# Kernel optimization log

Measured on AMD Instinct MI355X. Metric: run time of the kernel, lower is better.

Reference implementation:

```python
import jax, jax.numpy as jnp
import numpy as np

B, NQ, NKV, D, H = 2, 2048, 2048, 2048, 16
HD = D // H


def setup_inputs() -> dict:
    key = jax.random.key(0)
    ks = jax.random.split(key, 9)
    return {
        "x": jax.random.normal(ks[0], (B, NQ, D), jnp.float32),
        "k": jax.random.normal(ks[1], (B, H, NKV, HD), jnp.float32),
        "v": jax.random.normal(ks[2], (B, H, NKV, HD), jnp.float32),
        "tier_labels": jax.random.randint(ks[3], (B, NKV), 0, 3),
        "padding_mask": jnp.zeros((B, NKV), dtype=bool),
        "q_w": jax.random.normal(ks[4], (D, D), jnp.float32) * (D ** -0.5),
        "q_b": jax.random.normal(ks[5], (D,), jnp.float32) * 0.02,
        "out_w": jax.random.normal(ks[6], (D, D), jnp.float32) * (D ** -0.5),
        "out_b": jax.random.normal(ks[7], (D,), jnp.float32) * 0.02,
        "tier_bias": jax.random.normal(ks[8], (3,), jnp.float32) * 0.1,
    }


def reference(x, k, v, tier_labels, padding_mask, q_w, q_b, out_w, out_b, tier_bias):
    b, n_q, d = x.shape
    h, n_kv, hd = k.shape[1], k.shape[2], k.shape[3]
    scale = hd ** -0.5
    # q projection: torch Linear is x @ W.T + b
    q = x @ q_w.T + q_b                         # [b, n_q, d]
    q = q.reshape(b, n_q, h, hd).transpose(0, 2, 1, 3)  # [b, h, n_q, hd]
    attn = jnp.einsum("bhqd,bhkd->bhqk", q, k) * scale  # [b, h, n_q, n_kv]
    # additive tier bias gathered per kv token
    attn = attn + tier_bias[tier_labels][:, None, None, :]
    # causal mask: triu(-inf, diagonal=n_kv - n_q + 1)
    causal = jnp.triu(jnp.full((n_q, n_kv), -jnp.inf, dtype=x.dtype), k=n_kv - n_q + 1)
    attn = attn + causal
    # padding mask -> -inf
    attn = jnp.where(padding_mask[:, None, None, :], -jnp.inf, attn)
    attn = jax.nn.softmax(attn, axis=-1)
    out = jnp.einsum("bhqk,bhkd->bhqd", attn, v)  # [b, h, n_q, hd]
    out = out.transpose(0, 2, 1, 3).reshape(b, n_q, d)
    return out @ out_w.T + out_b
```

## Files before the change

kernel.cpp:

```cpp
#include <hip/hip_runtime.h>
#include <stdint.h>

typedef unsigned short u16;
typedef __attribute__((ext_vector_type(8))) short short8;
typedef __attribute__((ext_vector_type(4))) float f32x4;
typedef __attribute__((ext_vector_type(4))) uint32_t u32x4;

#define B_   2
#define NQ_  2048
#define NKV_ 2048
#define D_   2048
#define H_   16
#define HD_  128
#define MM_  (B_*NQ_)
#define LOG2E 1.4426950408889634f
#define QSCALE (0.08838834764831845f * 1.4426950408889634f)

__device__ __forceinline__ u16 f2bf(float f) {
  uint32_t u = __float_as_uint(f);
  u += 0x7fffu + ((u >> 16) & 1u);
  return (u16)(u >> 16);
}

__device__ __forceinline__ uint32_t cvtpk(float lo, float hi) {
  uint32_t r;
  asm("v_cvt_pk_bf16_f32 %0, %1, %2" : "=v"(r) : "v"(lo), "v"(hi));
  return r;
}

__device__ __forceinline__ void gload_lds16(const void* g, void* l) {
  __builtin_amdgcn_global_load_lds(
      (const __attribute__((address_space(1))) void*)g,
      (__attribute__((address_space(3))) void*)l, 16, 0, 0);
}

__global__ __launch_bounds__(256) void cast_all(
    const float* __restrict__ x,  const float* __restrict__ qw,
    const float* __restrict__ ow, const float* __restrict__ k,
    const float* __restrict__ v,
    u16* __restrict__ xo, u16* __restrict__ qwo, u16* __restrict__ owo,
    u16* __restrict__ ko, u16* __restrict__ vo)
{
  int i = blockIdx.x * 256 + threadIdx.x;
  const float* s; u16* d; int off;
  if      (i < 1048576) { s = x;  d = xo;  off = i; }
  else if (i < 1572864) { s = qw; d = qwo; off = i - 1048576; }
  else if (i < 2097152) { s = ow; d = owo; off = i - 1572864; }
  else if (i < 3145728) { s = k;  d = ko;  off = i - 2097152; }
  else                  { s = v;  d = vo;  off = i - 3145728; }
  const float4* sp = (const float4*)s + (size_t)off * 2;
  float4 a = sp[0], b = sp[1];
  short8 o;
  o[0] = (short)f2bf(a.x); o[1] = (short)f2bf(a.y);
  o[2] = (short)f2bf(a.z); o[3] = (short)f2bf(a.w);
  o[4] = (short)f2bf(b.x); o[5] = (short)f2bf(b.y);
  o[6] = (short)f2bf(b.z); o[7] = (short)f2bf(b.w);
  *((short8*)d + off) = o;
}

__global__ __launch_bounds__(256) void build_bias(const int* __restrict__ labels,
                                                  const unsigned char* __restrict__ mask,
                                                  const float* __restrict__ tb,
                                                  float* __restrict__ out, int n) {
  int i = blockIdx.x * 256 + threadIdx.x;
  if (i < n) out[i] = mask[i] ? -1e30f : tb[labels[i]] * LOG2E;
}

template<int OUT_BF16>
__global__ __launch_bounds__(256, 2) void gemm_bt(
    const u16* __restrict__ A, const u16* __restrict__ W,
    const float* __restrict__ bias, void* __restrict__ Cout,
    int M, int N, int K, float escale)
{
  __shared__ u16 As[2][128 * 64];
  __shared__ u16 Bs[2][128 * 64];
  const int tid = threadIdx.x;
  const int w = tid >> 6, l = tid & 63;
  const int lr = l & 15, lg = l >> 4;
  const int nbn = N >> 7;
  const int nwg = gridDim.x;
  int bid = blockIdx.x;
  int swz = (bid & 7) * (nwg >> 3) + (bid >> 3);
  const int bm = swz / nbn, bn = swz % nbn;
  const int wm = w >> 1, wn = w & 1;

  f32x4 acc[4][4] = {};

  const int sr = w * 32 + (l >> 3);
  const int sc = l & 7;

  auto stage = [&](int buf, int kt) {
#pragma unroll
    for (int i = 0; i < 4; ++i) {
      int r = sr + i * 8;
      int gc = kt + ((sc ^ (r & 7)) << 3);
      gload_lds16(A + (size_t)(bm * 128 + r) * K + gc,
                  (char*)&As[buf][0] + (w * 32 + i * 8) * 128);
      gload_lds16(W + (size_t)(bn * 128 + r) * K + gc,
                  (char*)&Bs[buf][0] + (w * 32 + i * 8) * 128);
    }
  };

  auto compute = [&](int buf) {
#pragma unroll
    for (int ks = 0; ks < 2; ++ks) {
      short8 av[4], bv[4];
#pragma unroll
      for (int mf = 0; mf < 4; ++mf) {
        int row = wm * 64 + mf * 16 + lr;
        int pch = (ks * 4 + lg) ^ (row & 7);
        av[mf] = *(const short8*)((const char*)&As[buf][0] + row * 128 + pch * 16);
      }
#pragma unroll
      for (int nf = 0; nf < 4; ++nf) {
        int row = wn * 64 + nf * 16 + lr;
        int pch = (ks * 4 + lg) ^ (row & 7);
        bv[nf] = *(const short8*)((const char*)&Bs[buf][0] + row * 128 + pch * 16);
      }
#pragma unroll
      for (int mf = 0; mf < 4; ++mf)
#pragma unroll
        for (int nf = 0; nf < 4; ++nf)
          acc[mf][nf] = __builtin_amdgcn_mfma_f32_16x16x32_bf16(av[mf], bv[nf], acc[mf][nf], 0, 0, 0);
    }
  };

  stage(0, 0);
  __syncthreads();
  int cur = 0;
  const int NT = K >> 6;
  for (int t = 0; t < NT - 1; ++t) {
    stage(cur ^ 1, (t + 1) << 6);
    compute(cur);
    __syncthreads();
    cur ^= 1;
  }
  compute(cur);

  const int row0 = bm * 128 + wm * 64;
  const int col0 = bn * 128 + wn * 64;
#pragma unroll
  for (int nf = 0; nf < 4; ++nf) {
    int col = col0 + nf * 16 + lr;
    float bb = bias[col];
#pragma unroll
    for (int mf = 0; mf < 4; ++mf) {
#pragma unroll
      for (int r = 0; r < 4; ++r) {
        size_t row = (size_t)(row0 + mf * 16 + lg * 4 + r);
        float vv = (acc[mf][nf][r] + bb) * escale;
        if (OUT_BF16) ((u16*)Cout)[row * N + col] = f2bf(vv);
        else          ((float*)Cout)[row * N + col] = vv;
      }
    }
  }
}

__device__ __forceinline__ void softmax16(
    const f32x4 s[4], const f32x4 bias4[4], bool diag, int qrow, int kv0,
    int lr, int lg, float& m, float& d, f32x4 o[8], short8 ap[2])
{
  float sv[4][4];
  float pm = -3e38f;
#pragma unroll
  for (int nf = 0; nf < 4; ++nf)
#pragma unroll
    for (int r = 0; r < 4; ++r) {
      float v = s[nf][r] + bias4[nf][r];
      if (diag) {
        int kv = kv0 + nf * 16 + lg * 4 + r;
        if (kv > qrow) v = -1e30f;
      }
      sv[nf][r] = v;
      pm = fmaxf(pm, v);
    }
  pm = fmaxf(pm, __shfl_xor(pm, 16));
  pm = fmaxf(pm, __shfl_xor(pm, 32));
  if (__any(pm > m + 8.f)) {
    float mn = fmaxf(m, pm);
    float al = __builtin_exp2f(m - mn);
    m = mn;
    d *= al;
    float alr[4];
#pragma unroll
    for (int r = 0; r < 4; ++r) alr[r] = __shfl(al, lg * 4 + r);
#pragma unroll
    for (int nf = 0; nf < 8; ++nf) {
      o[nf][0] *= alr[0]; o[nf][1] *= alr[1];
      o[nf][2] *= alr[2]; o[nf][3] *= alr[3];
    }
  }
  float ps = 0.f;
  uint32_t pk0[4], pk1[4];
#pragma unroll
  for (int nf = 0; nf < 4; ++nf) {
    float p0 = __builtin_exp2f(sv[nf][0] - m);
    float p1 = __builtin_exp2f(sv[nf][1] - m);
    float p2 = __builtin_exp2f(sv[nf][2] - m);
    float p3 = __builtin_exp2f(sv[nf][3] - m);
    ps += (p0 + p1) + (p2 + p3);
    pk0[nf] = cvtpk(p0, p1);
    pk1[nf] = cvtpk(p2, p3);
  }
  ps += __shfl_xor(ps, 16);
  ps += __shfl_xor(ps, 32);
  d += ps;
#pragma unroll
  for (int ks = 0; ks < 2; ++ks) {
    uint32_t rr[4];
#pragma unroll
    for (int i = 0; i < 4; ++i) {
      uint32_t c0 = ((lg & 1) == (i >> 1)) ? pk0[2 * ks] : pk0[2 * ks + 1];
      uint32_t c1 = ((lg & 1) == (i >> 1)) ? pk1[2 * ks] : pk1[2 * ks + 1];
      uint32_t contrib = (i & 1) ? c1 : c0;
      int srclg = (lg & 1) * 2 + ((i >> 1) ^ (lg >> 1));
      rr[i] = (uint32_t)__shfl((int)contrib, lr + 16 * srclg);
    }
    u32x4 t4;
    t4[0] = (lg & 2) ? rr[2] : rr[0];
    t4[1] = (lg & 2) ? rr[3] : rr[1];
    t4[2] = (lg & 2) ? rr[0] : rr[2];
    t4[3] = (lg & 2) ? rr[1] : rr[3];
    ap[ks] = __builtin_bit_cast(short8, t4);
  }
}

template<int WA>
__device__ __forceinline__ void compute_tile(
    const u16* __restrict__ ksb, const u16* __restrict__ vtb,
    const short8 aqB[4], const short8 aqA[4],
    f32x4 oB[8], f32x4 oA[8],
    float& mB, float& dB, float& mA, float& dA,
    const f32x4 bias4[4], bool diagB, bool diagA,
    int qrowB, int qrowA, int kv0, int lr, int lg)
{
  f32x4 sB[4] = {}, sA[4] = {};
  __builtin_amdgcn_s_setprio(1);
#pragma unroll
  for (int nf = 0; nf < 4; ++nf) {
#pragma unroll
    for (int ks = 0; ks < 4; ++ks) {
      int row = nf * 16 + lr;
      int pch = (ks * 4 + lg) ^ (row & 7);
      short8 bk = *(const short8*)((const char*)ksb + row * 256 + pch * 16);
      sB[nf] = __builtin_amdgcn_mfma_f32_16x16x32_bf16(bk, aqB[ks], sB[nf], 0, 0, 0);
      if (WA) sA[nf] = __builtin_amdgcn_mfma_f32_16x16x32_bf16(bk, aqA[ks], sA[nf], 0, 0, 0);
    }
  }
  __builtin_amdgcn_s_setprio(0);

  short8 apB[2], apA[2];
  softmax16(sB, bias4, diagB, qrowB, kv0, lr, lg, mB, dB, oB, apB);
  if (WA) softmax16(sA, bias4, diagA, qrowA, kv0, lr, lg, mA, dA, oA, apA);

  __builtin_amdgcn_s_setprio(1);
#pragma unroll
  for (int ks = 0; ks < 2; ++ks) {
#pragma unroll
    for (int nf = 0; nf < 8; ++nf) {
      int rowv = nf * 16 + lr;
      short8 bv = *(const short8*)(vtb + rowv * 64 + (((ks * 4 + lg) ^ (lr & 7)) << 3));
      oB[nf] = __builtin_amdgcn_mfma_f32_16x16x32_bf16(apB[ks], bv, oB[nf], 0, 0, 0);
      if (WA) oA[nf] = __builtin_amdgcn_mfma_f32_16x16x32_bf16(apA[ks], bv, oA[nf], 0, 0, 0);
    }
  }
  __builtin_amdgcn_s_setprio(0);
}

__global__ __launch_bounds__(256, 2) void attn_fwd(
    const u16* __restrict__ Q, const u16* __restrict__ Kg,
    const u16* __restrict__ Vg, const float* __restrict__ biaskv,
    u16* __restrict__ AO)
{
  __shared__ u16 Ks[2][64 * 128];
  __shared__ u16 Vt[2][128 * 64];

  const int tid = threadIdx.x;
  const int w = tid >> 6, l = tid & 63;
  const int lr = l & 15, lg = l >> 4;

  const int bid = blockIdx.x;
  const int bh = bid & 31, pi = bid >> 5;
  const int b = bh >> 4, h = bh & 15;
  const int qtA = pi, qtB = 31 - pi;

  const size_t kvbase = ((size_t)bh) * NKV_ * HD_;
  const u16* Kh = Kg + kvbase;
  const u16* Vh = Vg + kvbase;
  const float* bkv = biaskv + b * NKV_;

  const int q0A = qtA * 64 + w * 16;
  const int q0B = qtB * 64 + w * 16;

  short8 aqA[4], aqB[4];
  {
    const u16* qpA = Q + (size_t)(b * NQ_ + q0A + lr) * D_ + h * HD_ + lg * 8;
    const u16* qpB = Q + (size_t)(b * NQ_ + q0B + lr) * D_ + h * HD_ + lg * 8;
#pragma unroll
    for (int ks = 0; ks < 4; ++ks) {
      aqA[ks] = *(const short8*)(qpA + ks * 32);
      aqB[ks] = *(const short8*)(qpB + ks * 32);
    }
  }

  f32x4 oA[8] = {}, oB[8] = {};
  float mA = -1e30f, mB = -1e30f, dA = 0.f, dB = 0.f;

  short8 vv[4];
  {
#pragma unroll
    for (int i = 0; i < 4; ++i) {
      int r = w * 16 + i * 4 + lg;
      int c = lr ^ (r & 7);
      gload_lds16(Kh + (size_t)r * HD_ + c * 8, (char*)&Ks[0][0] + (w * 16 + i * 4) * 256);
    }
    const u16* vp = Vh + (size_t)l * HD_ + w * 32;
#pragma unroll
    for (int j = 0; j < 4; ++j) vv[j] = *(const short8*)(vp + j * 8);
#pragma unroll
    for (int j = 0; j < 4; ++j)
#pragma unroll
      for (int e = 0; e < 8; ++e) {
        int row = w * 32 + j * 8 + e;
        Vt[0][row * 64 + (((l >> 3) ^ (row & 7)) << 3) + (l & 7)] = (u16)vv[j][e];
      }
  }
  __syncthreads();

  int cur = 0;
  for (int kvt = 0; kvt <= qtB; ++kvt) {
    const int kv0 = kvt * 64;
    const bool haveNext = (kvt < qtB);
    if (haveNext) {
      const int kvn = kv0 + 64;
#pragma unroll
      for (int i = 0; i < 4; ++i) {
        int r = w * 16 + i * 4 + lg;
        int c = lr ^ (r & 7);
        gload_lds16(Kh + (size_t)(kvn + r) * HD_ + c * 8,
                    (char*)&Ks[cur ^ 1][0] + (w * 16 + i * 4) * 256);
      }
      const u16* vp = Vh + (size_t)(kvn + l) * HD_ + w * 32;
#pragma unroll
      for (int j = 0; j < 4; ++j) vv[j] = *(const short8*)(vp + j * 8);
    }

    f32x4 bias4[4];
#pragma unroll
    for (int nf = 0; nf < 4; ++nf)
      bias4[nf] = *(const f32x4*)(bkv + kv0 + nf * 16 + lg * 4);

    if (kvt <= qtA)
      compute_tile<1>(&Ks[cur][0], &Vt[cur][0], aqB, aqA, oB, oA, mB, dB, mA, dA,
                      bias4, kvt == qtB, kvt == qtA, q0B + lr, q0A + lr, kv0, lr, lg);
    else
      compute_tile<0>(&Ks[cur][0], &Vt[cur][0], aqB, aqA, oB, oA, mB, dB, mA, dA,
                      bias4, kvt == qtB, false, q0B + lr, q0A + lr, kv0, lr, lg);

    if (haveNext) {
#pragma unroll
      for (int j = 0; j < 4; ++j)
#pragma unroll
        for (int e = 0; e < 8; ++e) {
          int row = w * 32 + j * 8 + e;
          Vt[cur ^ 1][row * 64 + (((l >> 3) ^ (row & 7)) << 3) + (l & 7)] = (u16)vv[j][e];
        }
    }
    __syncthreads();
    cur ^= 1;
  }

  float dvB[4], dvA[4];
#pragma unroll
  for (int r = 0; r < 4; ++r) {
    dvB[r] = __shfl(dB, lg * 4 + r);
    dvA[r] = __shfl(dA, lg * 4 + r);
  }
#pragma unroll
  for (int r = 0; r < 4; ++r) {
    float inv = 1.f / dvB[r];
    size_t row = (size_t)(b * NQ_ + q0B + lg * 4 + r);
#pragma unroll
    for (int nf = 0; nf < 8; ++nf)
      AO[row * D_ + h * HD_ + nf * 16 + lr] = f2bf(oB[nf][r] * inv);
  }
#pragma unroll
  for (int r = 0; r < 4; ++r) {
    float inv = 1.f / dvA[r];
    size_t row = (size_t)(b * NQ_ + q0A + lg * 4 + r);
#pragma unroll
    for (int nf = 0; nf < 8; ++nf)
      AO[row * D_ + h * HD_ + nf * 16 + lr] = f2bf(oA[nf][r] * inv);
  }
}

extern "C" void kernel_launch(void* const* d_in, const int* in_sizes, int n_in,
                              void* d_out, int out_size, void* d_ws, size_t ws_size,
                              hipStream_t stream) {
  const float* x     = (const float*)d_in[0];
  const float* k     = (const float*)d_in[1];
  const float* v     = (const float*)d_in[2];
  const int*   labels = (const int*)d_in[3];
  const unsigned char* mask = (const unsigned char*)d_in[4];
  const float* q_w   = (const float*)d_in[5];
  const float* q_b   = (const float*)d_in[6];
  const float* out_w = (const float*)d_in[7];
  const float* out_b = (const float*)d_in[8];
  const float* tbias = (const float*)d_in[9];

  char* ws = (char*)d_ws;
  u16* x_bf  = (u16*)(ws + 0);
  u16* qw_bf = (u16*)(ws + 16777216);
  u16* ow_bf = (u16*)(ws + 25165824);
  u16* k_bf  = (u16*)(ws + 33554432);
  u16* v_bf  = (u16*)(ws + 50331648);
  u16* q_bf  = (u16*)(ws + 67108864);
  u16* ao_bf = (u16*)(ws + 83886080);
  float* bkv = (float*)(ws + 100663296);

  cast_all<<<16384, 256, 0, stream>>>(x, q_w, out_w, k, v,
                                      x_bf, qw_bf, ow_bf, k_bf, v_bf);
  build_bias<<<16, 256, 0, stream>>>(labels, mask, tbias, bkv, B_ * NKV_);

  gemm_bt<1><<<512, 256, 0, stream>>>(x_bf, qw_bf, q_b, (void*)q_bf, MM_, D_, D_, QSCALE);
  attn_fwd<<<512, 256, 0, stream>>>(q_bf, k_bf, v_bf, bkv, ao_bf);
  gemm_bt<0><<<512, 256, 0, stream>>>(ao_bf, ow_bf, out_b, d_out, MM_, D_, D_, 1.0f);
}
```

Baseline: 391.5 us.

## Rewrite projection GEMMs as 256x128-tile, 8-wave kernels with triple-buffered LDS pipeline

```diff
diff --git a/kernel.cpp b/kernel.cpp
--- a/kernel.cpp
+++ b/kernel.cpp
@@ -67,90 +67,95 @@
 }
 
 template<int OUT_BF16>
-__global__ __launch_bounds__(256, 2) void gemm_bt(
+__global__ __launch_bounds__(512, 2) void gemm8(
     const u16* __restrict__ A, const u16* __restrict__ W,
-    const float* __restrict__ bias, void* __restrict__ Cout,
-    int M, int N, int K, float escale)
+    const float* __restrict__ bias, void* __restrict__ Cout, float escale)
 {
-  __shared__ u16 As[2][128 * 64];
-  __shared__ u16 Bs[2][128 * 64];
+  __shared__ u16 Ah[6][128 * 64];
+  __shared__ u16 Bh[6][64 * 64];
   const int tid = threadIdx.x;
   const int w = tid >> 6, l = tid & 63;
   const int lr = l & 15, lg = l >> 4;
-  const int nbn = N >> 7;
-  const int nwg = gridDim.x;
+  const int wm = w >> 2, wn = w & 3;
   int bid = blockIdx.x;
-  int swz = (bid & 7) * (nwg >> 3) + (bid >> 3);
-  const int bm = swz / nbn, bn = swz % nbn;
-  const int wm = w >> 1, wn = w & 1;
-
-  f32x4 acc[4][4] = {};
-
-  const int sr = w * 32 + (l >> 3);
-  const int sc = l & 7;
-
-  auto stage = [&](int buf, int kt) {
-#pragma unroll
-    for (int i = 0; i < 4; ++i) {
-      int r = sr + i * 8;
-      int gc = kt + ((sc ^ (r & 7)) << 3);
-      gload_lds16(A + (size_t)(bm * 128 + r) * K + gc,
-                  (char*)&As[buf][0] + (w * 32 + i * 8) * 128);
-      gload_lds16(W + (size_t)(bn * 128 + r) * K + gc,
-                  (char*)&Bs[buf][0] + (w * 32 + i * 8) * 128);
+  int swz = (bid & 7) * 32 + (bid >> 3);
+  const int bm = swz >> 4, bn = swz & 15;
+
+  f32x4 acc[8][2] = {};
+
+  const int srl = l >> 3;
+  const int scl = l & 7;
+
+  auto stageA = [&](int t, int h) {
+#pragma unroll
+    for (int j = 0; j < 2; ++j) {
+      int r = w * 16 + j * 8 + srl;
+      int gc = t * 64 + ((scl ^ (r & 7)) << 3);
+      gload_lds16(A + (size_t)(bm * 256 + h * 128 + r) * 2048 + gc,
+                  &Ah[(2 * t + h) % 6][(w * 16 + j * 8) * 64]);
     }
   };
-
-  auto compute = [&](int buf) {
-#pragma unroll
-    for (int ks = 0; ks < 2; ++ks) {
-      short8 av[4], bv[4];
-#pragma unroll
-      for (int mf = 0; mf < 4; ++mf) {
-        int row = wm * 64 + mf * 16 + lr;
-        int pch = (ks * 4 + lg) ^ (row & 7);
-        av[mf] = *(const short8*)((const char*)&As[buf][0] + row * 128 + pch * 16);
-      }
-#pragma unroll
-      for (int nf = 0; nf < 4; ++nf) {
-        int row = wn * 64 + nf * 16 + lr;
-        int pch = (ks * 4 + lg) ^ (row & 7);
-        bv[nf] = *(const short8*)((const char*)&Bs[buf][0] + row * 128 + pch * 16);
-      }
-#pragma unroll
-      for (int mf = 0; mf < 4; ++mf)
-#pragma unroll
-        for (int nf = 0; nf < 4; ++nf)
-          acc[mf][nf] = __builtin_amdgcn_mfma_f32_16x16x32_bf16(av[mf], bv[nf], acc[mf][nf], 0, 0, 0);
-    }
+  auto stageB = [&](int t, int h) {
+    int r = w * 8 + srl;
+    int gc = t * 64 + ((scl ^ (r & 7)) << 3);
+    gload_lds16(W + (size_t)(bn * 128 + h * 64 + r) * 2048 + gc,
+                &Bh[(2 * t + h) % 6][(w * 8) * 64]);
   };
 
-  stage(0, 0);
-  __syncthreads();
-  int cur = 0;
-  const int NT = K >> 6;
-  for (int t = 0; t < NT - 1; ++t) {
-    stage(cur ^ 1, (t + 1) << 6);
-    compute(cur);
-    __syncthreads();
-    cur ^= 1;
-  }
-  compute(cur);
-
-  const int row0 = bm * 128 + wm * 64;
-  const int col0 = bn * 128 + wn * 64;
-#pragma unroll
-  for (int nf = 0; nf < 4; ++nf) {
-    int col = col0 + nf * 16 + lr;
+#define GPHASE(MH, VMSTR, DOSTAGE, t) do {                                     \
+    asm volatile(VMSTR ::: "memory");                                          \
+    __builtin_amdgcn_s_barrier();                                              \
+    __builtin_amdgcn_sched_barrier(0);                                         \
+    const u16* pa = &Ah[(2 * (t) + wm) % 6][0];                                \
+    const u16* pb = &Bh[(2 * (t) + (wn >> 1)) % 6][0];                         \
+    short8 av[4][2], bv[2][2];                                                 \
+    _Pragma("unroll") for (int mf = 0; mf < 4; ++mf) {                         \
+      int row = MH * 64 + mf * 16 + lr;                                        \
+      _Pragma("unroll") for (int ks = 0; ks < 2; ++ks) {                       \
+        int ch = (ks * 4 + lg) ^ (row & 7);                                    \
+        av[mf][ks] = *(const short8*)((const char*)pa + row * 128 + ch * 16);  \
+      } }                                                                      \
+    _Pragma("unroll") for (int nf = 0; nf < 2; ++nf) {                         \
+      int row = (wn & 1) * 32 + nf * 16 + lr;                                  \
+      _Pragma("unroll") for (int ks = 0; ks < 2; ++ks) {                       \
+        int ch = (ks * 4 + lg) ^ (row & 7);                                    \
+        bv[nf][ks] = *(const short8*)((const char*)pb + row * 128 + ch * 16);  \
+      } }                                                                      \
+    if (DOSTAGE) { stageA((t) + 2, MH); stageB((t) + 2, MH); }                 \
+    __builtin_amdgcn_s_setprio(1);                                             \
+    _Pragma("unroll") for (int mf = 0; mf < 4; ++mf)                           \
+      _Pragma("unroll") for (int nf = 0; nf < 2; ++nf)                         \
+        _Pragma("unroll") for (int ks = 0; ks < 2; ++ks)                       \
+          acc[MH * 4 + mf][nf] = __builtin_amdgcn_mfma_f32_16x16x32_bf16(      \
+              av[mf][ks], bv[nf][ks], acc[MH * 4 + mf][nf], 0, 0, 0);          \
+    __builtin_amdgcn_s_setprio(0);                                             \
+  } while (0)
+
+  stageA(0, 0); stageB(0, 0); stageA(0, 1); stageB(0, 1);
+  stageA(1, 0); stageB(1, 0); stageA(1, 1); stageB(1, 1);
+
+  for (int t = 0; t < 30; ++t) {
+    GPHASE(0, "s_waitcnt vmcnt(6)", 1, t);
+    GPHASE(1, "s_waitcnt vmcnt(9)", 1, t);
+  }
+  GPHASE(0, "s_waitcnt vmcnt(6)", 0, 30);
+  GPHASE(1, "s_waitcnt vmcnt(6)", 0, 30);
+  GPHASE(0, "s_waitcnt vmcnt(0)", 0, 31);
+  GPHASE(1, "s_waitcnt vmcnt(0)", 0, 31);
+#undef GPHASE
+
+#pragma unroll
+  for (int nf = 0; nf < 2; ++nf) {
+    int col = bn * 128 + wn * 32 + nf * 16 + lr;
     float bb = bias[col];
 #pragma unroll
-    for (int mf = 0; mf < 4; ++mf) {
+    for (int mfg = 0; mfg < 8; ++mfg) {
 #pragma unroll
       for (int r = 0; r < 4; ++r) {
-        size_t row = (size_t)(row0 + mf * 16 + lg * 4 + r);
-        float vv = (acc[mf][nf][r] + bb) * escale;
-        if (OUT_BF16) ((u16*)Cout)[row * N + col] = f2bf(vv);
-        else          ((float*)Cout)[row * N + col] = vv;
+        size_t row = (size_t)(bm * 256 + wm * 128 + mfg * 16 + lg * 4 + r);
+        float vv = (acc[mfg][nf][r] + bb) * escale;
+        if (OUT_BF16) ((u16*)Cout)[row * 2048 + col] = f2bf(vv);
+        else          ((float*)Cout)[row * 2048 + col] = vv;
       }
     }
   }
@@ -422,7 +427,7 @@
                                       x_bf, qw_bf, ow_bf, k_bf, v_bf);
   build_bias<<<16, 256, 0, stream>>>(labels, mask, tbias, bkv, B_ * NKV_);
 
-  gemm_bt<1><<<512, 256, 0, stream>>>(x_bf, qw_bf, q_b, (void*)q_bf, MM_, D_, D_, QSCALE);
+  gemm8<1><<<256, 512, 0, stream>>>(x_bf, qw_bf, q_b, (void*)q_bf, QSCALE);
   attn_fwd<<<512, 256, 0, stream>>>(q_bf, k_bf, v_bf, bkv, ao_bf);
-  gemm_bt<0><<<512, 256, 0, stream>>>(ao_bf, ow_bf, out_b, d_out, MM_, D_, D_, 1.0f);
-}
+  gemm8<0><<<256, 512, 0, stream>>>(ao_bf, ow_bf, out_b, d_out, 1.0f);
+}
```

After: 389.1 us. No clear change (-0.6%).

## Use 256x256 GEMM tiles and split attention q-tiles across 8-wave blocks

Applied to the files above, without the earlier changes.

```diff
diff --git a/kernel.cpp b/kernel.cpp
--- a/kernel.cpp
+++ b/kernel.cpp
@@ -67,90 +67,100 @@
 }
 
 template<int OUT_BF16>
-__global__ __launch_bounds__(256, 2) void gemm_bt(
+__global__ __launch_bounds__(512, 2) void gemm256(
     const u16* __restrict__ A, const u16* __restrict__ W,
-    const float* __restrict__ bias, void* __restrict__ Cout,
-    int M, int N, int K, float escale)
+    const float* __restrict__ bias, void* __restrict__ Cout, float escale)
 {
-  __shared__ u16 As[2][128 * 64];
-  __shared__ u16 Bs[2][128 * 64];
+  __shared__ u16 As[2][256 * 64];
+  __shared__ u16 Bs[2][256 * 64];
   const int tid = threadIdx.x;
   const int w = tid >> 6, l = tid & 63;
   const int lr = l & 15, lg = l >> 4;
-  const int nbn = N >> 7;
-  const int nwg = gridDim.x;
+  const int wm = w >> 2, wn = w & 3;
   int bid = blockIdx.x;
-  int swz = (bid & 7) * (nwg >> 3) + (bid >> 3);
-  const int bm = swz / nbn, bn = swz % nbn;
-  const int wm = w >> 1, wn = w & 1;
-
-  f32x4 acc[4][4] = {};
-
-  const int sr = w * 32 + (l >> 3);
-  const int sc = l & 7;
+  int swz = (bid & 7) * 16 + (bid >> 3);
+  const int bm = swz >> 3, bn = swz & 7;
+
+  f32x4 acc[8][4] = {};
+
+  const int srow = tid >> 3;
+  const int sch  = tid & 7;
 
   auto stage = [&](int buf, int kt) {
 #pragma unroll
     for (int i = 0; i < 4; ++i) {
-      int r = sr + i * 8;
-      int gc = kt + ((sc ^ (r & 7)) << 3);
-      gload_lds16(A + (size_t)(bm * 128 + r) * K + gc,
-                  (char*)&As[buf][0] + (w * 32 + i * 8) * 128);
-      gload_lds16(W + (size_t)(bn * 128 + r) * K + gc,
-                  (char*)&Bs[buf][0] + (w * 32 + i * 8) * 128);
+      int r = srow + i * 64;
+      int gc = kt + ((sch ^ (r & 7)) << 3);
+      gload_lds16(A + (size_t)(bm * 256 + r) * 2048 + gc,
+                  (char*)&As[buf][0] + tid * 16 + i * 8192);
+      gload_lds16(W + (size_t)(bn * 256 + r) * 2048 + gc,
+                  (char*)&Bs[buf][0] + tid * 16 + i * 8192);
     }
   };
 
-  auto compute = [&](int buf) {
-#pragma unroll
-    for (int ks = 0; ks < 2; ++ks) {
-      short8 av[4], bv[4];
+  stage(0, 0);
+  int cur = 0;
+  for (int t = 0; t < 32; ++t) {
+    if (t < 31) {
+      stage(cur ^ 1, (t + 1) * 64);
+      asm volatile("s_waitcnt vmcnt(8)" ::: "memory");
+    } else {
+      asm volatile("s_waitcnt vmcnt(0)" ::: "memory");
+    }
+    __builtin_amdgcn_s_barrier();
+    __builtin_amdgcn_sched_barrier(0);
+
+    const char* pa = (const char*)&As[cur][0];
+    const char* pb = (const char*)&Bs[cur][0];
+    short8 bv[4][2];
+#pragma unroll
+    for (int nf = 0; nf < 4; ++nf) {
+      int row = wn * 64 + nf * 16 + lr;
+#pragma unroll
+      for (int ks = 0; ks < 2; ++ks) {
+        int ch = (ks * 4 + lg) ^ (row & 7);
+        bv[nf][ks] = *(const short8*)(pb + row * 128 + ch * 16);
+      }
+    }
+#pragma unroll
+    for (int mh = 0; mh < 2; ++mh) {
+      short8 av[4][2];
 #pragma unroll
       for (int mf = 0; mf < 4; ++mf) {
-        int row = wm * 64 + mf * 16 + lr;
-        int pch = (ks * 4 + lg) ^ (row & 7);
-        av[mf] = *(const short8*)((const char*)&As[buf][0] + row * 128 + pch * 16);
-      }
-#pragma unroll
-      for (int nf = 0; nf < 4; ++nf) {
-        int row = wn * 64 + nf * 16 + lr;
-        int pch = (ks * 4 + lg) ^ (row & 7);
-        bv[nf] = *(const short8*)((const char*)&Bs[buf][0] + row * 128 + pch * 16);
-      }
+        int row = wm * 128 + mh * 64 + mf * 16 + lr;
+#pragma unroll
+        for (int ks = 0; ks < 2; ++ks) {
+          int ch = (ks * 4 + lg) ^ (row & 7);
+          av[mf][ks] = *(const short8*)(pa + row * 128 + ch * 16);
+        }
+      }
+      __builtin_amdgcn_s_setprio(1);
 #pragma unroll
       for (int mf = 0; mf < 4; ++mf)
 #pragma unroll
         for (int nf = 0; nf < 4; ++nf)
-          acc[mf][nf] = __builtin_amdgcn_mfma_f32_16x16x32_bf16(av[mf], bv[nf], acc[mf][nf], 0, 0, 0);
-    }
-  };
-
-  stage(0, 0);
-  __syncthreads();
-  int cur = 0;
-  const int NT = K >> 6;
-  for (int t = 0; t < NT - 1; ++t) {
-    stage(cur ^ 1, (t + 1) << 6);
-    compute(cur);
-    __syncthreads();
+#pragma unroll
+          for (int ks = 0; ks < 2; ++ks)
+            acc[mh * 4 + mf][nf] = __builtin_amdgcn_mfma_f32_16x16x32_bf16(
+                av[mf][ks], bv[nf][ks], acc[mh * 4 + mf][nf], 0, 0, 0);
+      __builtin_amdgcn_s_setprio(0);
+    }
+    __builtin_amdgcn_s_barrier();
     cur ^= 1;
   }
-  compute(cur);
-
-  const int row0 = bm * 128 + wm * 64;
-  const int col0 = bn * 128 + wn * 64;
+
 #pragma unroll
   for (int nf = 0; nf < 4; ++nf) {
-    int col = col0 + nf * 16 + lr;
+    int col = bn * 256 + wn * 64 + nf * 16 + lr;
     float bb = bias[col];
 #pragma unroll
-    for (int mf = 0; mf < 4; ++mf) {
+    for (int mfg = 0; mfg < 8; ++mfg) {
 #pragma unroll
       for (int r = 0; r < 4; ++r) {
-        size_t row = (size_t)(row0 + mf * 16 + lg * 4 + r);
-        float vv = (acc[mf][nf][r] + bb) * escale;
-        if (OUT_BF16) ((u16*)Cout)[row * N + col] = f2bf(vv);
-        else          ((float*)Cout)[row * N + col] = vv;
+        size_t row = (size_t)(bm * 256 + wm * 128 + mfg * 16 + lg * 4 + r);
+        float vv = (acc[mfg][nf][r] + bb) * escale;
+        if (OUT_BF16) ((u16*)Cout)[row * 2048 + col] = f2bf(vv);
+        else          ((float*)Cout)[row * 2048 + col] = vv;
       }
     }
   }
@@ -225,49 +235,7 @@
   }
 }
 
-template<int WA>
-__device__ __forceinline__ void compute_tile(
-    const u16* __restrict__ ksb, const u16* __restrict__ vtb,
-    const short8 aqB[4], const short8 aqA[4],
-    f32x4 oB[8], f32x4 oA[8],
-    float& mB, float& dB, float& mA, float& dA,
-    const f32x4 bias4[4], bool diagB, bool diagA,
-    int qrowB, int qrowA, int kv0, int lr, int lg)
-{
-  f32x4 sB[4] = {}, sA[4] = {};
-  __builtin_amdgcn_s_setprio(1);
-#pragma unroll
-  for (int nf = 0; nf < 4; ++nf) {
-#pragma unroll
-    for (int ks = 0; ks < 4; ++ks) {
-      int row = nf * 16 + lr;
-      int pch = (ks * 4 + lg) ^ (row & 7);
-      short8 bk = *(const short8*)((const char*)ksb + row * 256 + pch * 16);
-      sB[nf] = __builtin_amdgcn_mfma_f32_16x16x32_bf16(bk, aqB[ks], sB[nf], 0, 0, 0);
-      if (WA) sA[nf] = __builtin_amdgcn_mfma_f32_16x16x32_bf16(bk, aqA[ks], sA[nf], 0, 0, 0);
-    }
-  }
-  __builtin_amdgcn_s_setprio(0);
-
-  short8 apB[2], apA[2];
-  softmax16(sB, bias4, diagB, qrowB, kv0, lr, lg, mB, dB, oB, apB);
-  if (WA) softmax16(sA, bias4, diagA, qrowA, kv0, lr, lg, mA, dA, oA, apA);
-
-  __builtin_amdgcn_s_setprio(1);
-#pragma unroll
-  for (int ks = 0; ks < 2; ++ks) {
-#pragma unroll
-    for (int nf = 0; nf < 8; ++nf) {
-      int rowv = nf * 16 + lr;
-      short8 bv = *(const short8*)(vtb + rowv * 64 + (((ks * 4 + lg) ^ (lr & 7)) << 3));
-      oB[nf] = __builtin_amdgcn_mfma_f32_16x16x32_bf16(apB[ks], bv, oB[nf], 0, 0, 0);
-      if (WA) oA[nf] = __builtin_amdgcn_mfma_f32_16x16x32_bf16(apA[ks], bv, oA[nf], 0, 0, 0);
-    }
-  }
-  __builtin_amdgcn_s_setprio(0);
-}
-
-__global__ __launch_bounds__(256, 2) void attn_fwd(
+__global__ __launch_bounds__(512, 4) void attn_fwd(
     const u16* __restrict__ Q, const u16* __restrict__ Kg,
     const u16* __restrict__ Vg, const float* __restrict__ biaskv,
     u16* __restrict__ AO)
@@ -278,119 +246,119 @@
   const int tid = threadIdx.x;
   const int w = tid >> 6, l = tid & 63;
   const int lr = l & 15, lg = l >> 4;
+  const int sw = w >> 2;
+  const int wq = w & 3;
 
   const int bid = blockIdx.x;
   const int bh = bid & 31, pi = bid >> 5;
   const int b = bh >> 4, h = bh & 15;
   const int qtA = pi, qtB = 31 - pi;
+  const int myqt = sw ? qtA : qtB;
 
   const size_t kvbase = ((size_t)bh) * NKV_ * HD_;
   const u16* Kh = Kg + kvbase;
   const u16* Vh = Vg + kvbase;
   const float* bkv = biaskv + b * NKV_;
 
-  const int q0A = qtA * 64 + w * 16;
-  const int q0B = qtB * 64 + w * 16;
-
-  short8 aqA[4], aqB[4];
+  const int q0 = myqt * 64 + wq * 16;
+  short8 aq[4];
   {
-    const u16* qpA = Q + (size_t)(b * NQ_ + q0A + lr) * D_ + h * HD_ + lg * 8;
-    const u16* qpB = Q + (size_t)(b * NQ_ + q0B + lr) * D_ + h * HD_ + lg * 8;
-#pragma unroll
-    for (int ks = 0; ks < 4; ++ks) {
-      aqA[ks] = *(const short8*)(qpA + ks * 32);
-      aqB[ks] = *(const short8*)(qpB + ks * 32);
-    }
-  }
-
-  f32x4 oA[8] = {}, oB[8] = {};
-  float mA = -1e30f, mB = -1e30f, dA = 0.f, dB = 0.f;
-
-  short8 vv[4];
-  {
-#pragma unroll
-    for (int i = 0; i < 4; ++i) {
-      int r = w * 16 + i * 4 + lg;
-      int c = lr ^ (r & 7);
-      gload_lds16(Kh + (size_t)r * HD_ + c * 8, (char*)&Ks[0][0] + (w * 16 + i * 4) * 256);
-    }
-    const u16* vp = Vh + (size_t)l * HD_ + w * 32;
-#pragma unroll
-    for (int j = 0; j < 4; ++j) vv[j] = *(const short8*)(vp + j * 8);
-#pragma unroll
-    for (int j = 0; j < 4; ++j)
+    const u16* qp = Q + (size_t)(b * NQ_ + q0 + lr) * D_ + h * HD_ + lg * 8;
+#pragma unroll
+    for (int ks = 0; ks < 4; ++ks) aq[ks] = *(const short8*)(qp + ks * 32);
+  }
+
+  f32x4 o[8] = {};
+  float m = -1e30f, d = 0.f;
+
+  short8 vv[2];
+  auto stageK = [&](int buf, int kv) {
+#pragma unroll
+    for (int i = 0; i < 2; ++i) {
+      int r = (tid >> 4) + i * 32;
+      int c = (tid & 15) ^ (r & 7);
+      gload_lds16(Kh + (size_t)(kv + r) * HD_ + c * 8,
+                  (char*)&Ks[buf][0] + tid * 16 + i * 8192);
+    }
+  };
+  auto loadV = [&](int kv) {
+    const u16* vp = Vh + (size_t)(kv + l) * HD_ + w * 16;
+#pragma unroll
+    for (int j = 0; j < 2; ++j) vv[j] = *(const short8*)(vp + j * 8);
+  };
+  auto scatterV = [&](int buf) {
+#pragma unroll
+    for (int j = 0; j < 2; ++j)
 #pragma unroll
       for (int e = 0; e < 8; ++e) {
-        int row = w * 32 + j * 8 + e;
-        Vt[0][row * 64 + (((l >> 3) ^ (row & 7)) << 3) + (l & 7)] = (u16)vv[j][e];
-      }
-  }
+        int row = w * 16 + j * 8 + e;
+        Vt[buf][row * 64 + (((l >> 3) ^ (row & 7)) << 3) + (l & 7)] = (u16)vv[j][e];
+      }
+  };
+
+  stageK(0, 0);
+  loadV(0);
+  scatterV(0);
   __syncthreads();
 
   int cur = 0;
   for (int kvt = 0; kvt <= qtB; ++kvt) {
     const int kv0 = kvt * 64;
     const bool haveNext = (kvt < qtB);
-    if (haveNext) {
-      const int kvn = kv0 + 64;
-#pragma unroll
-      for (int i = 0; i < 4; ++i) {
-        int r = w * 16 + i * 4 + lg;
-        int c = lr ^ (r & 7);
-        gload_lds16(Kh + (size_t)(kvn + r) * HD_ + c * 8,
-                    (char*)&Ks[cur ^ 1][0] + (w * 16 + i * 4) * 256);
-      }
-      const u16* vp = Vh + (size_t)(kvn + l) * HD_ + w * 32;
-#pragma unroll
-      for (int j = 0; j < 4; ++j) vv[j] = *(const short8*)(vp + j * 8);
-    }
-
-    f32x4 bias4[4];
-#pragma unroll
-    for (int nf = 0; nf < 4; ++nf)
-      bias4[nf] = *(const f32x4*)(bkv + kv0 + nf * 16 + lg * 4);
-
-    if (kvt <= qtA)
-      compute_tile<1>(&Ks[cur][0], &Vt[cur][0], aqB, aqA, oB, oA, mB, dB, mA, dA,
-                      bias4, kvt == qtB, kvt == qtA, q0B + lr, q0A + lr, kv0, lr, lg);
-    else
-      compute_tile<0>(&Ks[cur][0], &Vt[cur][0], aqB, aqA, oB, oA, mB, dB, mA, dA,
-                      bias4, kvt == qtB, false, q0B + lr, q0A + lr, kv0, lr, lg);
-
-    if (haveNext) {
-#pragma unroll
-      for (int j = 0; j < 4; ++j)
-#pragma unroll
-        for (int e = 0; e < 8; ++e) {
-          int row = w * 32 + j * 8 + e;
-          Vt[cur ^ 1][row * 64 + (((l >> 3) ^ (row & 7)) << 3) + (l & 7)] = (u16)vv[j][e];
+    if (haveNext) { stageK(cur ^ 1, kv0 + 64); loadV(kv0 + 64); }
+
+    const bool active = (kvt <= myqt);
+    if (active) {
+      f32x4 bias4[4];
+#pragma unroll
+      for (int nf = 0; nf < 4; ++nf)
+        bias4[nf] = *(const f32x4*)(bkv + kv0 + nf * 16 + lg * 4);
+
+      f32x4 s[4] = {};
+      __builtin_amdgcn_s_setprio(1);
+#pragma unroll
+      for (int nf = 0; nf < 4; ++nf) {
+#pragma unroll
+        for (int ks = 0; ks < 4; ++ks) {
+          int row = nf * 16 + lr;
+          int pch = (ks * 4 + lg) ^ (row & 7);
+          short8 bk = *(const short8*)((const char*)&Ks[cur][0] + row * 256 + pch * 16);
+          s[nf] = __builtin_amdgcn_mfma_f32_16x16x32_bf16(bk, aq[ks], s[nf], 0, 0, 0);
         }
-    }
+      }
+      __builtin_amdgcn_s_setprio(0);
+
+      short8 ap[2];
+      softmax16(s, bias4, kvt == myqt, q0 + lr, kv0, lr, lg, m, d, o, ap);
+
+      __builtin_amdgcn_s_setprio(1);
+#pragma unroll
+      for (int ks = 0; ks < 2; ++ks) {
+#pragma unroll
+        for (int nf = 0; nf < 8; ++nf) {
+          int rowv = nf * 16 + lr;
+          short8 bv = *(const short8*)(&Vt[cur][0] + rowv * 64 + (((ks * 4 + lg) ^ (lr & 7)) << 3));
+          o[nf] = __builtin_amdgcn_mfma_f32_16x16x32_bf16(ap[ks], bv, o[nf], 0, 0, 0);
+        }
+      }
+      __builtin_amdgcn_s_setprio(0);
+    }
+
+    if (haveNext) scatterV(cur ^ 1);
     __syncthreads();
     cur ^= 1;
   }
 
-  float dvB[4], dvA[4];
+  float dv[4];
+#pragma unroll
+  for (int r = 0; r < 4; ++r) dv[r] = __shfl(d, lg * 4 + r);
 #pragma unroll
   for (int r = 0; r < 4; ++r) {
-    dvB[r] = __shfl(dB, lg * 4 + r);
-    dvA[r] = __shfl(dA, lg * 4 + r);
-  }
-#pragma unroll
-  for (int r = 0; r < 4; ++r) {
-    float inv = 1.f / dvB[r];
-    size_t row = (size_t)(b * NQ_ + q0B + lg * 4 + r);
+    float inv = 1.f / dv[r];
+    size_t row = (size_t)(b * NQ_ + q0 + lg * 4 + r);
 #pragma unroll
     for (int nf = 0; nf < 8; ++nf)
-      AO[row * D_ + h * HD_ + nf * 16 + lr] = f2bf(oB[nf][r] * inv);
-  }
-#pragma unroll
-  for (int r = 0; r < 4; ++r) {
-    float inv = 1.f / dvA[r];
-    size_t row = (size_t)(b * NQ_ + q0A + lg * 4 + r);
-#pragma unroll
-    for (int nf = 0; nf < 8; ++nf)
-      AO[row * D_ + h * HD_ + nf * 16 + lr] = f2bf(oA[nf][r] * inv);
+      AO[row * D_ + h * HD_ + nf * 16 + lr] = f2bf(o[nf][r] * inv);
   }
 }
 
@@ -422,7 +390,7 @@
                                       x_bf, qw_bf, ow_bf, k_bf, v_bf);
   build_bias<<<16, 256, 0, stream>>>(labels, mask, tbias, bkv, B_ * NKV_);
 
-  gemm_bt<1><<<512, 256, 0, stream>>>(x_bf, qw_bf, q_b, (void*)q_bf, MM_, D_, D_, QSCALE);
-  attn_fwd<<<512, 256, 0, stream>>>(q_bf, k_bf, v_bf, bkv, ao_bf);
-  gemm_bt<0><<<512, 256, 0, stream>>>(ao_bf, ow_bf, out_b, d_out, MM_, D_, D_, 1.0f);
-}
+  gemm256<1><<<128, 512, 0, stream>>>(x_bf, qw_bf, q_b, (void*)q_bf, QSCALE);
+  attn_fwd<<<512, 512, 0, stream>>>(q_bf, k_bf, v_bf, bkv, ao_bf);
+  gemm256<0><<<128, 512, 0, stream>>>(ao_bf, ow_bf, out_b, d_out, 1.0f);
+}
```

After: 432.1 us. 1.1x slower.
